# Kernel tuning notes

Measured on AMD Instinct MI355X. Metric: run time of the kernel, lower is better.

The kernel has to match this reference:

```python
import jax, jax.numpy as jnp
import numpy as np

ALPHA = 0.25
GAMMA = 2.0
SCALE = 32.0   # distance scale applied to raw uniform loc preds / ltrb targets
EPS = 1e-6

LEVEL_SHAPES = [(100, 128), (50, 64), (25, 32), (13, 16), (7, 8)]
B, C = 16, 80


def setup_inputs() -> dict:
    key = jax.random.key(0)
    ks = jax.random.split(key, 32)
    inp = {}
    for l, (H, W) in enumerate(LEVEL_SHAPES):
        k = jax.random.split(ks[l], 6)
        inp[f"conf{l}"] = jax.random.uniform(k[0], (B, C, H, W), jnp.float32)
        inp[f"loc{l}"] = jax.random.uniform(k[1], (B, 4, H, W), jnp.float32)
        inp[f"center{l}"] = jax.random.uniform(k[2], (B, 1, H, W), jnp.float32)
        inp[f"ltrb{l}"] = jax.random.uniform(k[3], (B, 4, H, W), jnp.float32)
        inp[f"cls{l}"] = jax.random.randint(k[4], (B, H, W), 0, C, jnp.int32)
        inp[f"pos{l}"] = jax.random.randint(k[5], (B, H, W), 0, 20, jnp.int32)
    return inp


def _level_losses(conf, loc, center, ltrb, cls, posraw):
    # conf: [B,C,H,W], loc/ltrb: [B,4,H,W], center: [B,1,H,W], cls/posraw: [B,H,W]
    pos_mask = posraw == 0                       # positive pixels
    p = jnp.clip(conf, 1e-8, 0.99999999)
    # focal loss: negative term everywhere, positive term at (cls, i, j) of positives
    neg = -(1.0 - ALPHA) * p ** GAMMA * jnp.log(1.0 - p)
    pos = -ALPHA * (1.0 - p) ** GAMMA * jnp.log(p)
    ch = jnp.arange(conf.shape[1], dtype=cls.dtype)[None, :, None, None]
    hit = pos_mask[:, None] & (ch == cls[:, None])   # [B,C,H,W]
    loss_conf = jnp.where(hit, pos, neg).sum(axis=(1, 2, 3))  # [B]

    # IoU loss (pred & target boxes share the pixel anchor -> coords cancel)
    lp, tp, rp, bp = jnp.moveaxis(loc * SCALE, 1, 0)
    lt, tt, rt, bt = jnp.moveaxis(ltrb * SCALE, 1, 0)
    iw = jnp.maximum(jnp.minimum(lp, lt) + jnp.minimum(rp, rt), 0.0)
    ih = jnp.maximum(jnp.minimum(tp, tt) + jnp.minimum(bp, bt), 0.0)
    inter = iw * ih
    area_p = jnp.maximum(lp + rp, 0.0) * jnp.maximum(tp + bp, 0.0)
    area_t = (lt + rt) * (tt + bt)
    iou = inter / (area_p + area_t - inter + EPS)
    iou_loss = -jnp.log(iou + EPS)
    loss_l = jnp.where(pos_mask, iou_loss, 0.0).sum(axis=(1, 2))  # [B]

    # centerness BCE: target = sqrt(min(l,r)/max(l,r) * min(t,b)/max(t,b))
    ctr_t = jnp.sqrt((jnp.minimum(lt, rt) / (jnp.maximum(lt, rt) + EPS)) *
                     (jnp.minimum(tt, bt) / (jnp.maximum(tt, bt) + EPS)))
    cp = jnp.clip(center[:, 0], 1e-8, 1.0 - 1e-8)
    bce = -(ctr_t * jnp.log(cp) + (1.0 - ctr_t) * jnp.log(1.0 - cp))
    loss_center = jnp.where(pos_mask, bce, 0.0).sum(axis=(1, 2))  # [B]

    poses = pos_mask.sum(axis=(1, 2))  # [B] int
    return loss_conf, loss_l, loss_center, poses


def reference(conf0, conf1, conf2, conf3, conf4,
              loc0, loc1, loc2, loc3, loc4,
              center0, center1, center2, center3, center4,
              ltrb0, ltrb1, ltrb2, ltrb3, ltrb4,
              cls0, cls1, cls2, cls3, cls4,
              pos0, pos1, pos2, pos3, pos4):
    confs = [conf0, conf1, conf2, conf3, conf4]
    locs = [loc0, loc1, loc2, loc3, loc4]
    centers = [center0, center1, center2, center3, center4]
    ltrbs = [ltrb0, ltrb1, ltrb2, ltrb3, ltrb4]
    clss = [cls0, cls1, cls2, cls3, cls4]
    poss = [pos0, pos1, pos2, pos3, pos4]

    loss_conf = jnp.zeros((B,), jnp.float32)
    loss_l = jnp.zeros((B,), jnp.float32)
    loss_center = jnp.zeros((B,), jnp.float32)
    poses = jnp.zeros((B,), jnp.int32)
    for l in range(5):  # fixed 5 FPN levels
        lc, ll, lctr, np_ = _level_losses(confs[l], locs[l], centers[l],
                                          ltrbs[l], clss[l], poss[l])
        loss_conf += lc
        loss_l += ll
        loss_center += lctr
        poses += np_

    posf = poses.astype(jnp.float32)
    per_img = jnp.where(poses > 0,
                        loss_center + (loss_conf + loss_l) / jnp.maximum(posf, 1.0),
                        loss_center + loss_conf + loss_l)
    return per_img.mean()
```

## Files before the change

### kernel.cpp

```cpp
#include <hip/hip_runtime.h>


namespace {
constexpr int NQUAD  = 4266;
constexpr int C_     = 80;
constexpr int CCHUNK = 10;
constexpr int GX     = 17;
constexpr float LN2  = 0.6931471805599453f;
constexpr float KNEG = -0.75f * LN2;
constexpr float KPOS = -0.25f * LN2;

struct LevelPtrs {
    const float* conf[5];
    const float* loc[5];
    const float* center[5];
    const float* ltrb[5];
    const int*   cls[5];
    const int*   pos[5];
};
}

__device__ __forceinline__ float flog2(float x) { return __builtin_amdgcn_logf(x); }

__device__ __forceinline__ float neg_term(float v) {
    float p = fminf(fmaxf(v, 1e-8f), 0.99999999f);
    return KNEG * p * p * flog2(1.f - p);
}
__device__ __forceinline__ float pos_term(float v) {
    float p = fminf(fmaxf(v, 1e-8f), 0.99999999f);
    float om = 1.f - p;
    return KPOS * om * om * flog2(p);
}

__global__ __launch_bounds__(256) void fcos_main(LevelPtrs P,
                                                 float* __restrict__ pc,
                                                 float* __restrict__ pl,
                                                 float* __restrict__ pcen,
                                                 int* __restrict__ pn) {
    const int b  = blockIdx.y;
    const int z  = blockIdx.z;
    const int c0 = z * CCHUNK;
    const int q  = blockIdx.x * 256 + threadIdx.x;

    float s_conf = 0.f, s_l = 0.f, s_c = 0.f;
    int s_n = 0;

    if (q < NQUAD) {
        int l, p, HW;
        if (q < 3200)      { l = 0; p = 4 * q;          HW = 12800; }
        else if (q < 4000) { l = 1; p = 4 * (q - 3200); HW = 3200; }
        else if (q < 4200) { l = 2; p = 4 * (q - 4000); HW = 800; }
        else if (q < 4252) { l = 3; p = 4 * (q - 4200); HW = 208; }
        else               { l = 4; p = 4 * (q - 4252); HW = 56; }

        const size_t bHW = (size_t)b * HW;
        const int4 cls4 = *(const int4*)(P.cls[l] + bHW + p);
        const int4 pos4 = *(const int4*)(P.pos[l] + bHW + p);
        const int clsA[4] = {cls4.x, cls4.y, cls4.z, cls4.w};
        const int posA[4] = {pos4.x, pos4.y, pos4.z, pos4.w};

        const float* confp = P.conf[l] + ((size_t)b * C_ + c0) * HW + p;
        float4 sc = make_float4(0.f, 0.f, 0.f, 0.f);
#pragma unroll
        for (int cc = 0; cc < CCHUNK; ++cc) {
            float4 v = *(const float4*)(confp + (size_t)cc * HW);
            sc.x += neg_term(v.x);
            sc.y += neg_term(v.y);
            sc.z += neg_term(v.z);
            sc.w += neg_term(v.w);
        }
        s_conf = (sc.x + sc.y) + (sc.z + sc.w);

#pragma unroll
        for (int i = 0; i < 4; ++i) {
            if (posA[i] == 0 && clsA[i] >= c0 && clsA[i] < c0 + CCHUNK) {
                float v = P.conf[l][((size_t)b * C_ + clsA[i]) * HW + p + i];
                s_conf += pos_term(v) - neg_term(v);
            }
        }

        if (z == 0) {
            const bool any = (posA[0] == 0) | (posA[1] == 0) |
                             (posA[2] == 0) | (posA[3] == 0);
            if (any) {
                const float* locp = P.loc[l]  + (size_t)b * 4 * HW + p;
                const float* ltrp = P.ltrb[l] + (size_t)b * 4 * HW + p;
                float la[4], ta[4], ra[4], ba[4];
                float La[4], Ta[4], Ra[4], Ba[4];
                float ca[4];
                *(float4*)la = *(const float4*)(locp);
                *(float4*)ta = *(const float4*)(locp + HW);
                *(float4*)ra = *(const float4*)(locp + 2 * HW);
                *(float4*)ba = *(const float4*)(locp + 3 * HW);
                *(float4*)La = *(const float4*)(ltrp);
                *(float4*)Ta = *(const float4*)(ltrp + HW);
                *(float4*)Ra = *(const float4*)(ltrp + 2 * HW);
                *(float4*)Ba = *(const float4*)(ltrp + 3 * HW);
                *(float4*)ca = *(const float4*)(P.center[l] + bHW + p);
#pragma unroll
                for (int i = 0; i < 4; ++i) {
                    if (posA[i] != 0) continue;
                    float lp = la[i] * 32.f, tp = ta[i] * 32.f,
                          rp = ra[i] * 32.f, bp = ba[i] * 32.f;
                    float lt = La[i] * 32.f, tt = Ta[i] * 32.f,
                          rt = Ra[i] * 32.f, bt = Ba[i] * 32.f;

                    float iw = fmaxf(fminf(lp, lt) + fminf(rp, rt), 0.f);
                    float ih = fmaxf(fminf(tp, tt) + fminf(bp, bt), 0.f);
                    float inter  = iw * ih;
                    float area_p = fmaxf(lp + rp, 0.f) * fmaxf(tp + bp, 0.f);
                    float area_t = (lt + rt) * (tt + bt);
                    float iou = inter / (area_p + area_t - inter + 1e-6f);
                    s_l += -LN2 * flog2(iou + 1e-6f);

                    float ctr = sqrtf((fminf(lt, rt) / (fmaxf(lt, rt) + 1e-6f)) *
                                      (fminf(tt, bt) / (fmaxf(tt, bt) + 1e-6f)));
                    float cp = fminf(fmaxf(ca[i], 1e-8f), 1.f - 1e-8f);
                    s_c += -LN2 * (ctr * flog2(cp) + (1.f - ctr) * flog2(1.f - cp));
                    s_n += 1;
                }
            }
        }
    }

    for (int o = 32; o > 0; o >>= 1) {
        s_conf += __shfl_down(s_conf, o, 64);
        if (z == 0) {
            s_l += __shfl_down(s_l, o, 64);
            s_c += __shfl_down(s_c, o, 64);
            s_n += __shfl_down(s_n, o, 64);
        }
    }

    __shared__ float redc[4], redl[4], redcen[4];
    __shared__ int redn[4];
    const int wid = threadIdx.x >> 6;
    if ((threadIdx.x & 63) == 0) {
        redc[wid] = s_conf; redl[wid] = s_l; redcen[wid] = s_c; redn[wid] = s_n;
    }
    __syncthreads();
    if (threadIdx.x == 0) {
        float tc = (redc[0] + redc[1]) + (redc[2] + redc[3]);
        pc[((size_t)b * 8 + z) * GX + blockIdx.x] = tc;
        if (z == 0) {
            pl[b * GX + blockIdx.x]   = (redl[0] + redl[1]) + (redl[2] + redl[3]);
            pcen[b * GX + blockIdx.x] = (redcen[0] + redcen[1]) + (redcen[2] + redcen[3]);
            pn[b * GX + blockIdx.x]   = redn[0] + redn[1] + redn[2] + redn[3];
        }
    }
}

__global__ __launch_bounds__(1024) void fcos_final(const float* __restrict__ pc,
                                                   const float* __restrict__ pl,
                                                   const float* __restrict__ pcen,
                                                   const int* __restrict__ pn,
                                                   float* __restrict__ out) {
    const int tid  = threadIdx.x;
    const int b    = tid >> 6;
    const int lane = tid & 63;

    float sc = 0.f, sl = 0.f, scen = 0.f;
    int sn = 0;
    for (int i = lane; i < 8 * GX; i += 64) sc += pc[b * 8 * GX + i];
    if (lane < GX) {
        sl   = pl[b * GX + lane];
        scen = pcen[b * GX + lane];
        sn   = pn[b * GX + lane];
    }
    for (int o = 32; o > 0; o >>= 1) {
        sc   += __shfl_down(sc, o, 64);
        sl   += __shfl_down(sl, o, 64);
        scen += __shfl_down(scen, o, 64);
        sn   += __shfl_down(sn, o, 64);
    }

    __shared__ float vals[16];
    if (lane == 0) {
        float pf = fmaxf((float)sn, 1.f);
        vals[b] = (sn > 0) ? (scen + (sc + sl) / pf) : (scen + sc + sl);
    }
    __syncthreads();
    if (tid == 0) {
        float s = 0.f;
        for (int i = 0; i < 16; ++i) s += vals[i];
        out[0] = s * (1.f / 16.f);
    }
}

extern "C" void kernel_launch(void* const* d_in, const int* in_sizes, int n_in,
                              void* d_out, int out_size, void* d_ws, size_t ws_size,
                              hipStream_t stream) {
    LevelPtrs P;
    for (int l = 0; l < 5; ++l) {
        P.conf[l]   = (const float*)d_in[l * 6 + 0];
        P.loc[l]    = (const float*)d_in[l * 6 + 1];
        P.center[l] = (const float*)d_in[l * 6 + 2];
        P.ltrb[l]   = (const float*)d_in[l * 6 + 3];
        P.cls[l]    = (const int*)d_in[l * 6 + 4];
        P.pos[l]    = (const int*)d_in[l * 6 + 5];
    }
    float* pc   = (float*)d_ws;
    float* pl   = pc + 16 * 8 * GX;
    float* pcen = pl + 16 * GX;
    int*   pn   = (int*)(pcen + 16 * GX);

    dim3 grid(GX, 16, 8);
    fcos_main<<<grid, 256, 0, stream>>>(P, pc, pl, pcen, pn);
    fcos_final<<<1, 1024, 0, stream>>>(pc, pl, pcen, pn, (float*)d_out);
}
```

Measured before the change: 168.6 us.

## Split box/centerness loss into separate z-slice and buffer conf loads in registers

Adds a ninth z-slice of blocks dedicated to IoU and centerness losses, so the z==0 conf blocks no longer carry the extra box work and load imbalance. Conf loads for the channel chunk are issued up front into a register array to increase memory-level parallelism. The positive-class term reuses the buffered value instead of issuing another global load. This costs more registers per thread and an extra set of blocks, each of which reloads cls/pos.

```diff
diff --git a/kernel.cpp b/kernel.cpp
--- a/kernel.cpp
+++ b/kernel.cpp
@@ -32,54 +32,65 @@
     return KPOS * om * om * flog2(p);
 }
 
+__device__ __forceinline__ void level_of(int q, int& l, int& p, int& HW) {
+    if (q < 3200)      { l = 0; p = 4 * q;          HW = 12800; }
+    else if (q < 4000) { l = 1; p = 4 * (q - 3200); HW = 3200; }
+    else if (q < 4200) { l = 2; p = 4 * (q - 4000); HW = 800; }
+    else if (q < 4252) { l = 3; p = 4 * (q - 4200); HW = 208; }
+    else               { l = 4; p = 4 * (q - 4252); HW = 56; }
+}
+
 __global__ __launch_bounds__(256) void fcos_main(LevelPtrs P,
                                                  float* __restrict__ pc,
                                                  float* __restrict__ pl,
                                                  float* __restrict__ pcen,
                                                  int* __restrict__ pn) {
-    const int b  = blockIdx.y;
-    const int z  = blockIdx.z;
-    const int c0 = z * CCHUNK;
-    const int q  = blockIdx.x * 256 + threadIdx.x;
+    const int b = blockIdx.y;
+    const int z = blockIdx.z;
+    const int q = blockIdx.x * 256 + threadIdx.x;
 
     float s_conf = 0.f, s_l = 0.f, s_c = 0.f;
     int s_n = 0;
+    const bool is_box = (z == 8);
 
     if (q < NQUAD) {
         int l, p, HW;
-        if (q < 3200)      { l = 0; p = 4 * q;          HW = 12800; }
-        else if (q < 4000) { l = 1; p = 4 * (q - 3200); HW = 3200; }
-        else if (q < 4200) { l = 2; p = 4 * (q - 4000); HW = 800; }
-        else if (q < 4252) { l = 3; p = 4 * (q - 4200); HW = 208; }
-        else               { l = 4; p = 4 * (q - 4252); HW = 56; }
-
+        level_of(q, l, p, HW);
         const size_t bHW = (size_t)b * HW;
         const int4 cls4 = *(const int4*)(P.cls[l] + bHW + p);
         const int4 pos4 = *(const int4*)(P.pos[l] + bHW + p);
         const int clsA[4] = {cls4.x, cls4.y, cls4.z, cls4.w};
         const int posA[4] = {pos4.x, pos4.y, pos4.z, pos4.w};
 
-        const float* confp = P.conf[l] + ((size_t)b * C_ + c0) * HW + p;
-        float4 sc = make_float4(0.f, 0.f, 0.f, 0.f);
-#pragma unroll
-        for (int cc = 0; cc < CCHUNK; ++cc) {
-            float4 v = *(const float4*)(confp + (size_t)cc * HW);
-            sc.x += neg_term(v.x);
-            sc.y += neg_term(v.y);
-            sc.z += neg_term(v.z);
-            sc.w += neg_term(v.w);
-        }
-        s_conf = (sc.x + sc.y) + (sc.z + sc.w);
-
-#pragma unroll
-        for (int i = 0; i < 4; ++i) {
-            if (posA[i] == 0 && clsA[i] >= c0 && clsA[i] < c0 + CCHUNK) {
-                float v = P.conf[l][((size_t)b * C_ + clsA[i]) * HW + p + i];
-                s_conf += pos_term(v) - neg_term(v);
+        if (!is_box) {
+            const int c0 = z * CCHUNK;
+            const float* confp = P.conf[l] + ((size_t)b * C_ + c0) * HW + p;
+
+            float4 vb[CCHUNK];
+#pragma unroll
+            for (int cc = 0; cc < CCHUNK; ++cc)
+                vb[cc] = *(const float4*)(confp + (size_t)cc * HW);
+
+            float4 sc = make_float4(0.f, 0.f, 0.f, 0.f);
+#pragma unroll
+            for (int cc = 0; cc < CCHUNK; ++cc) {
+                sc.x += neg_term(vb[cc].x);
+                sc.y += neg_term(vb[cc].y);
+                sc.z += neg_term(vb[cc].z);
+                sc.w += neg_term(vb[cc].w);
             }
-        }
-
-        if (z == 0) {
+            s_conf = (sc.x + sc.y) + (sc.z + sc.w);
+
+#pragma unroll
+            for (int i = 0; i < 4; ++i) {
+                if (posA[i] == 0 && clsA[i] >= c0 && clsA[i] < c0 + CCHUNK) {
+                    float v = vb[clsA[i] - c0].x;
+                    const float* vf = (const float*)&vb[clsA[i] - c0];
+                    v = vf[i];
+                    s_conf += pos_term(v) - neg_term(v);
+                }
+            }
+        } else {
             const bool any = (posA[0] == 0) | (posA[1] == 0) |
                              (posA[2] == 0) | (posA[3] == 0);
             if (any) {
@@ -123,9 +134,10 @@
         }
     }
 
-    for (int o = 32; o > 0; o >>= 1) {
-        s_conf += __shfl_down(s_conf, o, 64);
-        if (z == 0) {
+    if (!is_box) {
+        for (int o = 32; o > 0; o >>= 1) s_conf += __shfl_down(s_conf, o, 64);
+    } else {
+        for (int o = 32; o > 0; o >>= 1) {
             s_l += __shfl_down(s_l, o, 64);
             s_c += __shfl_down(s_c, o, 64);
             s_n += __shfl_down(s_n, o, 64);
@@ -140,9 +152,10 @@
     }
     __syncthreads();
     if (threadIdx.x == 0) {
-        float tc = (redc[0] + redc[1]) + (redc[2] + redc[3]);
-        pc[((size_t)b * 8 + z) * GX + blockIdx.x] = tc;
-        if (z == 0) {
+        if (!is_box) {
+            pc[((size_t)b * 8 + z) * GX + blockIdx.x] =
+                (redc[0] + redc[1]) + (redc[2] + redc[3]);
+        } else {
             pl[b * GX + blockIdx.x]   = (redl[0] + redl[1]) + (redl[2] + redl[3]);
             pcen[b * GX + blockIdx.x] = (redcen[0] + redcen[1]) + (redcen[2] + redcen[3]);
             pn[b * GX + blockIdx.x]   = redn[0] + redn[1] + redn[2] + redn[3];
@@ -204,7 +217,7 @@
     float* pcen = pl + 16 * GX;
     int*   pn   = (int*)(pcen + 16 * GX);
 
-    dim3 grid(GX, 16, 8);
+    dim3 grid(GX, 16, 9);
     fcos_main<<<grid, 256, 0, stream>>>(P, pc, pl, pcen, pn);
     fcos_final<<<1, 1024, 0, stream>>>(pc, pl, pcen, pn, (float*)d_out);
 }
```

After: 201.9 us. 1.2x slower.
